# Kernel optimization log

Measured on AMD Instinct MI355X. Metric: run time of the kernel, lower is better.

## Reference

```python
import jax, jax.numpy as jnp
import numpy as np

ALPHA = 0.25
GAMMA = 2.0
PROB_MIN = 0.0001


def _gather_feat(feat, inds):
    # feat: [B, C, H, W], inds: [B, K] in [0, H*W) -> [B, K, C]
    B, C, H, W = feat.shape
    f = feat.reshape(B, C, H * W).transpose(0, 2, 1)  # [B, HW, C]
    return jnp.take_along_axis(f, inds[:, :, None], axis=1)


def setup_inputs() -> dict:
    key = jax.random.key(0)
    ks = jax.random.split(key, 7)
    B, C, H, W, K = 8, 64, 152, 272, 500
    HW = H * W
    cur_reid = jax.random.normal(ks[0], (B, C, H, W), dtype=jnp.float32)
    pre_reid = jax.random.normal(ks[1], (B, C, H, W), dtype=jnp.float32)
    cur_inds = jax.random.randint(ks[2], (B, K), 0, HW, dtype=jnp.int64)
    pre_inds = jax.random.randint(ks[3], (B, K), 0, HW, dtype=jnp.int64)
    cur_circum_ind = jax.random.randint(ks[4], (B, K), 0, HW, dtype=jnp.int64)
    pre_circum_ind = jax.random.randint(ks[5], (B, K), 0, HW, dtype=jnp.int64)
    tracking_mask = jax.random.randint(ks[6], (B, K, 1), 0, 2, dtype=jnp.int32)
    return {
        "cur_reid": cur_reid,
        "pre_reid": pre_reid,
        "cur_inds": cur_inds,
        "pre_inds": pre_inds,
        "cur_circum_ind": cur_circum_ind,
        "pre_circum_ind": pre_circum_ind,
        "tracking_mask": tracking_mask,
    }


def reference(cur_reid, pre_reid, cur_inds, pre_inds, cur_circum_ind, pre_circum_ind, tracking_mask):
    mask = tracking_mask[:, :, 0].astype(jnp.int64)  # [B, K], 0/1
    # Replace indices of non-tracked slots with the pre-drawn random indices
    cur_idx = cur_inds * mask + cur_circum_ind * (1 - mask)
    pre_idx = pre_inds * mask + pre_circum_ind * (1 - mask)

    cur_feat = _gather_feat(cur_reid, cur_idx)  # [B, K, C]
    pre_feat = _gather_feat(pre_reid, pre_idx)  # [B, K, C]

    # similarity[b, i, j] = sigmoid(<cur_feat[b,i], pre_feat[b,j]>)
    sim = jax.nn.sigmoid(jnp.einsum("bic,bjc->bij", cur_feat, pre_feat))  # [B, K, K]

    # groundtruth = diag_embed(mask): gt[b,i,i] = mask[b,i]
    K = mask.shape[1]
    gt = mask[:, :, None] * jnp.eye(K, dtype=mask.dtype)[None]  # [B, K, K]

    # focal loss: p_t = sim if gt==1 else 1-sim; alpha_t = 0.25 if gt==1 else 0.75
    probs = jnp.where(gt == 1, sim, 1.0 - sim)
    probs = jnp.clip(probs, PROB_MIN, 1.0)
    alpha_t = jnp.where(gt == 1, ALPHA, 1.0 - ALPHA)
    loss = jnp.mean(-alpha_t * (1.0 - probs) ** GAMMA * jnp.log(probs))
    return loss
```

## Files before the change

### kernel.cpp

```cpp
#include <hip/hip_runtime.h>

#define B 8
#define C 64
#define H 152
#define W 272
#define HW (H * W)
#define K 500
#define KP 512
#define ALPHA 0.25f
#define PROB_MIN 1e-4f

typedef __attribute__((ext_vector_type(8))) short short8;
typedef __attribute__((ext_vector_type(4))) float floatx4;

__device__ __forceinline__ unsigned short f32_to_bf16(float f) {
    union { float f; unsigned int u; } v; v.f = f;
    unsigned int r = v.u + 0x7FFFu + ((v.u >> 16) & 1u);
    return (unsigned short)(r >> 16);
}

__global__ __launch_bounds__(128) void gather_kernel(
    const float* __restrict__ cur_reid,
    const float* __restrict__ pre_reid,
    const int* __restrict__ cur_inds,
    const int* __restrict__ pre_inds,
    const int* __restrict__ cur_circ,
    const int* __restrict__ pre_circ,
    const int* __restrict__ tmask,
    unsigned short* __restrict__ curf,
    unsigned short* __restrict__ pref,
    float* __restrict__ out)
{
    const int bk = blockIdx.x;
    const int t  = threadIdx.x;
    if (bk == 0 && t == 0) out[0] = 0.0f;

    const int b = bk >> 9;
    const int k = bk & (KP - 1);

    if (k >= K) {
        if (t < C)      curf[(size_t)bk * C + t] = 0;
        else            pref[(size_t)bk * C + (t - C)] = 0;
        return;
    }

    const int bk_in = b * K + k;
    const int m = tmask[bk_in];
    if (t < C) {
        const int idx = m ? cur_inds[bk_in] : cur_circ[bk_in];
        const float v = cur_reid[((size_t)(b * C + t)) * HW + idx];
        curf[(size_t)bk * C + t] = f32_to_bf16(v);
    } else {
        const int c = t - C;
        const int idx = m ? pre_inds[bk_in] : pre_circ[bk_in];
        const float v = pre_reid[((size_t)(b * C + c)) * HW + idx];
        pref[(size_t)bk * C + c] = f32_to_bf16(v);
    }
}

__device__ __forceinline__ float focal_term(float x, int gi, int gj, int b,
                                            const int* __restrict__ tmask)
{
    if (gi >= K || gj >= K) return 0.0f;
    const float sim = 1.0f / (1.0f + __expf(-x));
    const int gt = (gi == gj) ? tmask[b * K + gi] : 0;
    float p = gt ? sim : 1.0f - sim;
    p = fminf(fmaxf(p, PROB_MIN), 1.0f);
    const float a = gt ? ALPHA : (1.0f - ALPHA);
    const float om = 1.0f - p;
    return a * om * om * (-__logf(p));
}

#define LOSS_THREADS 1024

__global__ __launch_bounds__(LOSS_THREADS) void loss_kernel(
    const unsigned short* __restrict__ curf,
    const unsigned short* __restrict__ pref,
    const int* __restrict__ tmask,
    float* __restrict__ out)
{
    __shared__ float wsum[LOSS_THREADS / 64];

    const int t    = threadIdx.x;
    const int wave = t >> 6;
    const int lane = t & 63;

    const int tile = blockIdx.x * (LOSS_THREADS / 64) + wave;
    const int b    = tile >> 10;
    const int rem  = tile & 1023;
    const int ti   = rem >> 5;
    const int tj   = rem & 31;

    const int m16  = lane & 15;
    const int quad = lane >> 4;

    const unsigned short* pa = curf + (((size_t)(b * KP + ti * 16 + m16)) * C + quad * 8);
    const unsigned short* pb = pref + (((size_t)(b * KP + tj * 16 + m16)) * C + quad * 8);
    const short8 a0 = *(const short8*)pa;
    const short8 a1 = *(const short8*)(pa + 32);
    const short8 b0 = *(const short8*)pb;
    const short8 b1 = *(const short8*)(pb + 32);

    floatx4 acc = {0.f, 0.f, 0.f, 0.f};
    acc = __builtin_amdgcn_mfma_f32_16x16x32_bf16(a0, b0, acc, 0, 0, 0);
    acc = __builtin_amdgcn_mfma_f32_16x16x32_bf16(a1, b1, acc, 0, 0, 0);

    const int gj = tj * 16 + m16;
    float s = 0.f;
#pragma unroll
    for (int r = 0; r < 4; ++r) {
        const int gi = ti * 16 + quad * 4 + r;
        s += focal_term(acc[r], gi, gj, b, tmask);
    }

#pragma unroll
    for (int o = 32; o > 0; o >>= 1) s += __shfl_down(s, o, 64);
    if (lane == 0) wsum[wave] = s;
    __syncthreads();
    if (t == 0) {
        float tot = 0.f;
#pragma unroll
        for (int w = 0; w < LOSS_THREADS / 64; ++w) tot += wsum[w];
        atomicAdd(out, tot * (1.0f / ((float)B * (float)K * (float)K)));
    }
}

extern "C" void kernel_launch(void* const* d_in, const int* in_sizes, int n_in,
                              void* d_out, int out_size, void* d_ws, size_t ws_size,
                              hipStream_t stream)
{
    const float* cur_reid = (const float*)d_in[0];
    const float* pre_reid = (const float*)d_in[1];
    const int*   cur_inds = (const int*)d_in[2];
    const int*   pre_inds = (const int*)d_in[3];
    const int*   cur_circ = (const int*)d_in[4];
    const int*   pre_circ = (const int*)d_in[5];
    const int*   tmask    = (const int*)d_in[6];
    float*       out      = (float*)d_out;

    unsigned short* curf = (unsigned short*)d_ws;
    unsigned short* pref = curf + (size_t)B * KP * C;

    gather_kernel<<<B * KP, 128, 0, stream>>>(
        cur_reid, pre_reid, cur_inds, pre_inds, cur_circ, pre_circ, tmask,
        curf, pref, out);

    loss_kernel<<<512, LOSS_THREADS, 0, stream>>>(curf, pref, tmask, out);
}
```

Baseline: 176.4 us.

## Remap gather kernel to one block per channel plane with threads over K

The gather kernel now launches one block per (channel, batch, array) and has each thread fetch indices for up to two K slots, reading from a single channel plane. Before, each block handled one K slot across all channels, striding HW floats between threads. Each block's random reads now fall inside one plane, which may improve TLB and cache locality. The cost is that index and mask loads are repeated for every channel, and the bf16 writes are strided by C elements, so they no longer coalesce.

New measurement: 180.5 us. 1.02x slower.

```diff
diff --git a/kernel.cpp b/kernel.cpp
--- a/kernel.cpp
+++ b/kernel.cpp
@@ -19,7 +19,7 @@
     return (unsigned short)(r >> 16);
 }
 
-__global__ __launch_bounds__(128) void gather_kernel(
+__global__ __launch_bounds__(256) void gather_kernel(
     const float* __restrict__ cur_reid,
     const float* __restrict__ pre_reid,
     const int* __restrict__ cur_inds,
@@ -31,30 +31,29 @@
     unsigned short* __restrict__ pref,
     float* __restrict__ out)
 {
-    const int bk = blockIdx.x;
-    const int t  = threadIdx.x;
-    if (bk == 0 && t == 0) out[0] = 0.0f;
+    const int c   = blockIdx.x;
+    const int b   = blockIdx.y;
+    const int arr = blockIdx.z;
+    const int t   = threadIdx.x;
 
-    const int b = bk >> 9;
-    const int k = bk & (KP - 1);
+    if (c == 0 && b == 0 && arr == 0 && t == 0)
+        out[0] = 0.0f;
 
-    if (k >= K) {
-        if (t < C)      curf[(size_t)bk * C + t] = 0;
-        else            pref[(size_t)bk * C + (t - C)] = 0;
-        return;
-    }
+    const float* plane = (arr ? pre_reid : cur_reid) + ((size_t)(b * C + c)) * HW;
+    const int* inds = arr ? pre_inds : cur_inds;
+    const int* circ = arr ? pre_circ : cur_circ;
+    unsigned short* feat = arr ? pref : curf;
 
-    const int bk_in = b * K + k;
-    const int m = tmask[bk_in];
-    if (t < C) {
-        const int idx = m ? cur_inds[bk_in] : cur_circ[bk_in];
-        const float v = cur_reid[((size_t)(b * C + t)) * HW + idx];
-        curf[(size_t)bk * C + t] = f32_to_bf16(v);
-    } else {
-        const int c = t - C;
-        const int idx = m ? pre_inds[bk_in] : pre_circ[bk_in];
-        const float v = pre_reid[((size_t)(b * C + c)) * HW + idx];
-        pref[(size_t)bk * C + c] = f32_to_bf16(v);
+#pragma unroll
+    for (int r = 0; r < 2; ++r) {
+        const int k = t + r * 256;
+        unsigned short v = 0;
+        if (k < K) {
+            const int bk  = b * K + k;
+            const int idx = tmask[bk] ? inds[bk] : circ[bk];
+            v = f32_to_bf16(plane[idx]);
+        }
+        feat[((size_t)(b * KP + k)) * C + c] = v;
     }
 }
 
@@ -141,7 +140,8 @@
     unsigned short* curf = (unsigned short*)d_ws;
     unsigned short* pref = curf + (size_t)B * KP * C;
 
-    gather_kernel<<<B * KP, 128, 0, stream>>>(
+    dim3 ggrid(C, B, 2);
+    gather_kernel<<<ggrid, 256, 0, stream>>>(
         cur_reid, pre_reid, cur_inds, pre_inds, cur_circ, pre_circ, tmask,
         curf, pref, out);
 
```
